# Optimization experiments

Hardware: AMD Instinct MI355X
Metric: run time of the kernel (lower is better)

## Reference

```python
import jax, jax.numpy as jnp
import numpy as np
from jax import lax


def _conv1x1(x, w, b=None):
    # x: [N,C,H,W], w: [O,C]
    y = jnp.einsum('nchw,oc->nohw', x, w)
    if b is not None:
        y = y + b[None, :, None, None]
    return y


def _bn(x, g, b, rm, rv):
    # eval-mode BatchNorm2d, eps=1e-5 (torch default)
    inv = g / jnp.sqrt(rv + 1e-5)
    return x * inv[None, :, None, None] + (b - rm * inv)[None, :, None, None]


def setup_inputs() -> dict:
    key = jax.random.key(0)
    ks = jax.random.split(key, 32)
    N, C1, C2, H, W = 16, 256, 256, 64, 64
    mid = C2 // 16  # local_att reduction=16
    f32 = jnp.float32
    def nrm(k, shp, s=0.05):
        return s * jax.random.normal(k, shp, f32)
    return dict(
        x1=jax.random.normal(ks[0], (N, C1, H, W), f32),
        x2=jax.random.normal(ks[1], (N, C2, H, W), f32),
        conv1_w=nrm(ks[2], (C2, C1)), conv1_b=nrm(ks[3], (C2,)),
        conv2_w=nrm(ks[4], (C2, C2)), conv2_b=nrm(ks[5], (C2,)),
        conv3_w=nrm(ks[6], (C2, C2)), conv3_b=nrm(ks[7], (C2,)),
        conv4_w=nrm(ks[8], (C2, C2)), conv4_b=nrm(ks[9], (C2,)),
        conv4g_w=nrm(ks[10], (1, C2)), conv4g_b=nrm(ks[11], (1,)),
        bn_g=1.0 + nrm(ks[12], (C2,)), bn_b=nrm(ks[13], (C2,)),
        bn_rm=nrm(ks[14], (C2,)), bn_rv=1.0 + 0.1 * jax.random.uniform(ks[15], (C2,), f32),
        gamma=jax.random.normal(ks[16], (C2, 1, 1), f32), beta=jnp.zeros((C2, 1, 1), f32),
        gate_w=nrm(ks[17], (C2, C2)), gate_b=nrm(ks[18], (C2,)),
        dw_w=nrm(ks[19], (C2, 1, 3, 3)), dw_b=nrm(ks[20], (C2,)),
        interact_w=nrm(ks[21], (C2 // 4, C2 // 4)), interact_b=0.5 + nrm(ks[22], (C2 // 4,)),
        ca_w=nrm(ks[23], (1, 1, 5)),  # channel_att conv1d kernel, k=5 for C=256
        la1_w=nrm(ks[24], (mid, C2)),
        la_bn_g=1.0 + nrm(ks[25], (mid,)), la_bn_b=nrm(ks[26], (mid,)),
        la_bn_rm=nrm(ks[27], (mid,)), la_bn_rv=1.0 + 0.1 * jax.random.uniform(ks[28], (mid,), f32),
        fh_w=nrm(ks[29], (C2, mid)), fw_w=nrm(ks[30], (C2, mid)),
    )


def reference(x1, x2, conv1_w, conv1_b, conv2_w, conv2_b, conv3_w, conv3_b,
              conv4_w, conv4_b, conv4g_w, conv4g_b, bn_g, bn_b, bn_rm, bn_rv,
              gamma, beta, gate_w, gate_b, dw_w, dw_b, interact_w, interact_b,
              ca_w, la1_w, la_bn_g, la_bn_b, la_bn_rm, la_bn_rv, fh_w, fw_w):
    N, _, H, W = x1.shape
    C = conv1_w.shape[0]
    g1 = _conv1x1(x1, conv1_w, conv1_b)
    w1 = jax.nn.sigmoid(_bn(g1, bn_g, bn_b, bn_rm, bn_rv))
    g2 = _conv1x1(x2, conv2_w, conv2_b)
    w2 = jax.nn.sigmoid(_bn(g2, bn_g, bn_b, bn_rm, bn_rv))
    XG = g1 + g2

    # channel_att: GAP -> conv1d(k=5) across channels -> sigmoid gate
    y = XG.mean((2, 3))[:, None, :]  # [N,1,C]
    y = lax.conv_general_dilated(y, ca_w, (1,), [(2, 2)],
                                 dimension_numbers=('NCH', 'OIH', 'NCH'))
    temp = XG * jax.nn.sigmoid(y[:, 0, :])[:, :, None, None]

    # spatial sigmoid gate then 4-way group interact + softmax reweight
    Xs = jax.nn.sigmoid(_conv1x1(XG, conv4g_w, conv4g_b)) * XG
    C4 = C // 4
    Xr = Xs.reshape(N, 4, C4, H, W)
    o1 = jnp.einsum('ngchw,oc->ngohw', Xr, interact_w) + interact_b[None, None, :, None, None]
    xmap = o1.reshape(N, 4, 1, C4 * H * W)
    xav = xmap / xmap.mean(-1, keepdims=True)
    soft = jax.nn.softmax(xav, axis=2)  # softmax over size-1 dim -> ones (faithful)
    out = (soft.reshape(N, 4, C4, H, W) * Xr).reshape(N, C, H, W)

    # per-group (16) normalization using X_GOBAL stats (std unbiased, ddof=1)
    GN = 16
    xs = XG.reshape(N, GN, -1)
    mu = xs.mean(-1, keepdims=True)
    sd = jnp.std(xs, axis=-1, keepdims=True, ddof=1)
    x_gui = ((out.reshape(N, GN, -1) - mu) / (sd + 1e-10)).reshape(N, C, H, W)
    x_gui = x_gui * gamma[None] + beta[None]

    # threshold masks vs global-avg sigmoid reweights
    rw = jax.nn.sigmoid(XG.mean((2, 3), keepdims=True))  # [N,C,1,1]
    up1 = rw >= w1
    up2 = rw >= w2
    zero = jnp.zeros((), XG.dtype)
    x_up = jnp.where(up1, XG, zero) + jnp.where(up2, XG, zero)
    x_low = jnp.where(~up1, XG, zero) + jnp.where(~up2, XG, zero)

    # low branch: dwconv3x3 -> 1x1 -> channel-softmax gate
    dw = lax.conv_general_dilated(x_low, dw_w, (1, 1), [(1, 1), (1, 1)],
                                  dimension_numbers=('NCHW', 'OIHW', 'NCHW'),
                                  feature_group_count=C) + dw_b[None, :, None, None]
    x11 = _conv1x1(dw, conv3_w, conv3_b)
    gate = jax.nn.softmax(jax.nn.relu(x_low.mean((2, 3)) @ gate_w.T + gate_b), axis=1)
    xL = x11 * gate[:, :, None, None] + _conv1x1(x_up, conv4_w, conv4_b) + x_gui + temp

    # local_att (coordinate attention)
    xh = jnp.swapaxes(xL.mean(3, keepdims=True), 2, 3)  # [N,C,1,H]
    xw = xL.mean(2, keepdims=True)                       # [N,C,1,W]
    yc = jax.nn.relu(_bn(_conv1x1(jnp.concatenate([xh, xw], 3), la1_w),
                         la_bn_g, la_bn_b, la_bn_rm, la_bn_rv))
    sh = jax.nn.sigmoid(_conv1x1(jnp.swapaxes(yc[..., :H], 2, 3), fh_w))  # [N,C,H,1]
    sw = jax.nn.sigmoid(_conv1x1(yc[..., H:], fw_w))                      # [N,C,1,W]
    return xL * sh * sw
```

## Files before the change

### kernel.cpp

```cpp
#include <hip/hip_runtime.h>
#include <cstddef>
#include <cstdint>

constexpr int NN = 16, CC = 256, HH = 64, WW = 64, HW = 64 * 64;
constexpr size_t FSZ = (size_t)NN * CC * HW;

typedef short bf16x8 __attribute__((ext_vector_type(8)));
typedef float f32x4 __attribute__((ext_vector_type(4)));

__device__ __forceinline__ float sigmoidf_(float x) { return 1.f / (1.f + expf(-x)); }

__device__ __forceinline__ unsigned short bf16_rne(float f) {
    uint32_t u = __builtin_bit_cast(uint32_t, f);
    u += 0x7FFFu + ((u >> 16) & 1u);
    return (unsigned short)(u >> 16);
}
__device__ __forceinline__ float bf16_tof(unsigned short h) {
    uint32_t u = ((uint32_t)h) << 16;
    return __builtin_bit_cast(float, u);
}

__global__ __launch_bounds__(256) void wsplit_kernel(
    const float* __restrict__ w1, const float* __restrict__ w2,
    const float* __restrict__ w3, const float* __restrict__ w4,
    unsigned short* __restrict__ w1h, unsigned short* __restrict__ w1m, unsigned short* __restrict__ w1l,
    unsigned short* __restrict__ w2h, unsigned short* __restrict__ w2m, unsigned short* __restrict__ w2l,
    unsigned short* __restrict__ w4h, unsigned short* __restrict__ w4l,
    unsigned short* __restrict__ w3b) {
    const int i = blockIdx.x * 256 + threadIdx.x;
    {
        float x = w1[i];
        unsigned short h = bf16_rne(x); float r = x - bf16_tof(h);
        unsigned short m = bf16_rne(r); float r2 = r - bf16_tof(m);
        w1h[i] = h; w1m[i] = m; w1l[i] = bf16_rne(r2);
    }
    {
        float x = w2[i];
        unsigned short h = bf16_rne(x); float r = x - bf16_tof(h);
        unsigned short m = bf16_rne(r); float r2 = r - bf16_tof(m);
        w2h[i] = h; w2m[i] = m; w2l[i] = bf16_rne(r2);
    }
    {
        float x = w4[i];
        unsigned short h = bf16_rne(x); float r = x - bf16_tof(h);
        w4h[i] = h; w4l[i] = bf16_rne(r);
    }
    w3b[i] = bf16_rne(w3[i]);
}

template <int NS>
__global__ __launch_bounds__(256) void tsplit_kernel(const float* __restrict__ X,
                                                     unsigned short* __restrict__ O0,
                                                     unsigned short* __restrict__ O1,
                                                     unsigned short* __restrict__ O2) {
    const int hw0 = blockIdx.x * 64, c0 = blockIdx.y * 64, n = blockIdx.z;
    __shared__ float sT[64][65];
    const int tid = threadIdx.x;
    {
        const int hwl = (tid & 15) << 2;
        const int cl = tid >> 4;
#pragma unroll
        for (int p = 0; p < 4; ++p) {
            const int c = cl + p * 16;
            const float4 v = *(const float4*)(X + ((size_t)(n * CC + c0 + c)) * HW + hw0 + hwl);
            sT[c][hwl] = v.x; sT[c][hwl + 1] = v.y; sT[c][hwl + 2] = v.z; sT[c][hwl + 3] = v.w;
        }
    }
    __syncthreads();
    const int hwl = tid >> 2, cb = (tid & 3) << 4;
    unsigned short h[16], m[16], l[16];
#pragma unroll
    for (int j = 0; j < 16; ++j) {
        const float x = sT[cb + j][hwl];
        const unsigned short hh = bf16_rne(x);
        h[j] = hh;
        if (NS >= 2) {
            const float r = x - bf16_tof(hh);
            const unsigned short mm = bf16_rne(r);
            m[j] = mm;
            if (NS >= 3) l[j] = bf16_rne(r - bf16_tof(mm));
        }
    }
    const size_t ob = ((size_t)(n * HW + hw0 + hwl)) * 256 + c0 + cb;
    *(int4*)(O0 + ob) = *(int4*)&h[0]; *(int4*)(O0 + ob + 8) = *(int4*)&h[8];
    if (NS >= 2) { *(int4*)(O1 + ob) = *(int4*)&m[0]; *(int4*)(O1 + ob + 8) = *(int4*)&m[8]; }
    if (NS >= 3) { *(int4*)(O2 + ob) = *(int4*)&l[0]; *(int4*)(O2 + ob + 8) = *(int4*)&l[8]; }
}

template <int NS>
__device__ __forceinline__ void mfma_core(const unsigned short* X0,
                                          const unsigned short* X1,
                                          const unsigned short* X2,
                                          const unsigned short* W0,
                                          const unsigned short* W1,
                                          const unsigned short* W2,
                                          int n, int hw0, int o0, f32x4 acc[4]) {
    __shared__ unsigned short sX[NS][64][40];
    __shared__ unsigned short sW[NS][64][40];
    const int tid = threadIdx.x;
    const int row = tid >> 2, koff = (tid & 3) << 3;
    const int lane = tid & 63, wv = tid >> 6, quad = lane >> 4, nlo = lane & 15;
    const unsigned short* Xs[3] = {X0, X1, X2};
    const unsigned short* Ws[3] = {W0, W1, W2};
    const size_t xbase = ((size_t)(n * HW + hw0 + row)) * 256 + koff;
    const size_t wbase = ((size_t)(o0 + row)) * 256 + koff;
    for (int k0 = 0; k0 < 256; k0 += 32) {
#pragma unroll
        for (int s = 0; s < NS; ++s) {
            *(int4*)&sX[s][row][koff] = *(const int4*)(Xs[s] + xbase + k0);
            *(int4*)&sW[s][row][koff] = *(const int4*)(Ws[s] + wbase + k0);
        }
        __syncthreads();
        bf16x8 af[NS];
#pragma unroll
        for (int s = 0; s < NS; ++s) af[s] = *(const bf16x8*)&sW[s][wv * 16 + nlo][quad * 8];
#pragma unroll
        for (int nt = 0; nt < 4; ++nt) {
            bf16x8 bfr[NS];
#pragma unroll
            for (int s = 0; s < NS; ++s) bfr[s] = *(const bf16x8*)&sX[s][nt * 16 + nlo][quad * 8];
            if (NS == 3) {
                acc[nt] = __builtin_amdgcn_mfma_f32_16x16x32_bf16(af[1], bfr[1], acc[nt], 0, 0, 0);
                acc[nt] = __builtin_amdgcn_mfma_f32_16x16x32_bf16(af[0], bfr[2], acc[nt], 0, 0, 0);
                acc[nt] = __builtin_amdgcn_mfma_f32_16x16x32_bf16(af[2], bfr[0], acc[nt], 0, 0, 0);
                acc[nt] = __builtin_amdgcn_mfma_f32_16x16x32_bf16(af[0], bfr[1], acc[nt], 0, 0, 0);
                acc[nt] = __builtin_amdgcn_mfma_f32_16x16x32_bf16(af[1], bfr[0], acc[nt], 0, 0, 0);
                acc[nt] = __builtin_amdgcn_mfma_f32_16x16x32_bf16(af[0], bfr[0], acc[nt], 0, 0, 0);
            } else if (NS == 2) {
                acc[nt] = __builtin_amdgcn_mfma_f32_16x16x32_bf16(af[0], bfr[1], acc[nt], 0, 0, 0);
                acc[nt] = __builtin_amdgcn_mfma_f32_16x16x32_bf16(af[1], bfr[0], acc[nt], 0, 0, 0);
                acc[nt] = __builtin_amdgcn_mfma_f32_16x16x32_bf16(af[0], bfr[0], acc[nt], 0, 0, 0);
            } else {
                acc[nt] = __builtin_amdgcn_mfma_f32_16x16x32_bf16(af[0], bfr[0], acc[nt], 0, 0, 0);
            }
        }
        __syncthreads();
    }
}

template <int NS>
__global__ __launch_bounds__(256) void gemm_mfma_kernel(
    const unsigned short* __restrict__ X0, const unsigned short* __restrict__ X1,
    const unsigned short* __restrict__ X2, const unsigned short* __restrict__ W0,
    const unsigned short* __restrict__ W1, const unsigned short* __restrict__ W2,
    const float* __restrict__ bias, float* __restrict__ Y) {
    const int hw0 = blockIdx.x * 64, o0 = blockIdx.y * 64, n = blockIdx.z;
    f32x4 acc[4] = {};
    mfma_core<NS>(X0, X1, X2, W0, W1, W2, n, hw0, o0, acc);
    const int lane = threadIdx.x & 63, wv = threadIdx.x >> 6;
    const int quad = lane >> 4, nlo = lane & 15;
    const int om = o0 + wv * 16 + quad * 4;
#pragma unroll
    for (int nt = 0; nt < 4; ++nt) {
        const int hw = hw0 + nt * 16 + nlo;
#pragma unroll
        for (int r = 0; r < 4; ++r) {
            const int o = om + r;
            Y[((size_t)(n * CC + o)) * HW + hw] = acc[nt][r] + bias[o];
        }
    }
}

__global__ __launch_bounds__(256) void gemm_final_kernel(
    const unsigned short* __restrict__ X0, const unsigned short* __restrict__ W0,
    const float* __restrict__ bias,
    const float* A, const float* __restrict__ XG, const float* __restrict__ s_pix,
    const float* __restrict__ gate, const float* __restrict__ ca_sig,
    const float* __restrict__ mu_g, const float* __restrict__ isd_g,
    const float* __restrict__ gamma, const float* __restrict__ beta,
    float* out) {
    const int hw0 = blockIdx.x * 64, o0 = blockIdx.y * 64, n = blockIdx.z;
    f32x4 acc[4] = {};
    mfma_core<1>(X0, nullptr, nullptr, W0, nullptr, nullptr, n, hw0, o0, acc);
    const int lane = threadIdx.x & 63, wv = threadIdx.x >> 6;
    const int quad = lane >> 4, nlo = lane & 15;
    const int om = o0 + wv * 16 + quad * 4;
#pragma unroll
    for (int nt = 0; nt < 4; ++nt) {
        const int hw = hw0 + nt * 16 + nlo;
        const int pix = n * HW + hw;
        const float sp = s_pix[pix];
#pragma unroll
        for (int r = 0; r < 4; ++r) {
            const int o = om + r;
            const float g = gate[n * CC + o];
            const float cs = ca_sig[n * CC + o];
            const float mu = mu_g[n * 16 + (o >> 4)];
            const float isd = isd_g[n * 16 + (o >> 4)];
            const size_t rowi = ((size_t)(n * CC + o)) * HW + hw;
            const float xg = XG[rowi];
            const float gui = (sp * xg - mu) * isd * gamma[o] + beta[o];
            out[rowi] = (acc[nt][r] + bias[o]) * g + A[rowi] + gui + xg * cs;
        }
    }
}

__global__ __launch_bounds__(256) void xg_stats_kernel(const float* __restrict__ g1,
                                                       const float* __restrict__ g2,
                                                       float* __restrict__ XG,
                                                       float* __restrict__ sum_c,
                                                       float* __restrict__ sq_c) {
    const size_t base = (size_t)blockIdx.x * HW;
    float s = 0.f, q = 0.f;
#pragma unroll 4
    for (int r = 0; r < 16; ++r) {
        const size_t i = base + threadIdx.x + r * 256;
        const float xg = g1[i] + g2[i];
        XG[i] = xg;
        s += xg;
        q += xg * xg;
    }
    __shared__ float sm[8];
    for (int off = 32; off; off >>= 1) { s += __shfl_down(s, off); q += __shfl_down(q, off); }
    const int w = threadIdx.x >> 6;
    if ((threadIdx.x & 63) == 0) { sm[w] = s; sm[4 + w] = q; }
    __syncthreads();
    if (threadIdx.x == 0) {
        sum_c[blockIdx.x] = sm[0] + sm[1] + sm[2] + sm[3];
        sq_c[blockIdx.x] = sm[4] + sm[5] + sm[6] + sm[7];
    }
}

__global__ __launch_bounds__(256) void stats2_kernel(const float* __restrict__ sum_c,
                                                     const float* __restrict__ sq_c,
                                                     const float* __restrict__ caw,
                                                     float* __restrict__ rw,
                                                     float* __restrict__ ca_sig,
                                                     float* __restrict__ mu_g,
                                                     float* __restrict__ isd_g) {
    const int n = blockIdx.x, c = threadIdx.x;
    __shared__ float m[256];
    const float mean = sum_c[n * CC + c] * (1.f / (float)HW);
    m[c] = mean;
    rw[n * CC + c] = sigmoidf_(mean);
    __syncthreads();
    float y = 0.f;
#pragma unroll
    for (int k = 0; k < 5; ++k) {
        const int cc = c - 2 + k;
        if (cc >= 0 && cc < 256) y += m[cc] * caw[k];
    }
    ca_sig[n * CC + c] = sigmoidf_(y);
    if (c < 16) {
        float S = 0.f, Q = 0.f;
        for (int j = 0; j < 16; ++j) {
            S += sum_c[n * CC + c * 16 + j];
            Q += sq_c[n * CC + c * 16 + j];
        }
        const float cnt = 65536.f;
        const float mu = S / cnt;
        float var = (Q - S * S / cnt) * (1.f / (cnt - 1.f));
        var = fmaxf(var, 0.f);
        mu_g[n * 16 + c] = mu;
        isd_g[n * 16 + c] = 1.f / (sqrtf(var) + 1e-10f);
    }
}

__global__ __launch_bounds__(256) void conv4g_kernel(const float* __restrict__ XG,
                                                     const float* __restrict__ cgw,
                                                     const float* __restrict__ cgb,
                                                     float* __restrict__ s_pix) {
    __shared__ float w[256];
    w[threadIdx.x] = cgw[threadIdx.x];
    __syncthreads();
    const int p = blockIdx.x * 256 + threadIdx.x;
    const int n = p >> 12, hw = p & 4095;
    const float* base = XG + (size_t)n * CC * HW + hw;
    float s = cgb[0];
#pragma unroll 8
    for (int c = 0; c < 256; ++c) s += base[(size_t)c * HW] * w[c];
    s_pix[p] = sigmoidf_(s);
}

__global__ __launch_bounds__(256) void masks_kernel(float* g1_xlow,
                                                    const float* __restrict__ g2,
                                                    const float* __restrict__ XG,
                                                    const float* __restrict__ rw,
                                                    const float* __restrict__ bng,
                                                    const float* __restrict__ bnb,
                                                    const float* __restrict__ bnrm,
                                                    const float* __restrict__ bnrv,
                                                    float* __restrict__ xup,
                                                    float* __restrict__ xlow_sum) {
    const int nc = blockIdx.x;
    const int c = nc & 255;
    const float inv = bng[c] / sqrtf(bnrv[c] + 1e-5f);
    const float off = bnb[c] - bnrm[c] * inv;
    const float rwv = rw[nc];
    const size_t base = (size_t)nc * HW;
    float lsum = 0.f;
#pragma unroll 4
    for (int r = 0; r < 16; ++r) {
        const size_t i = base + threadIdx.x + r * 256;
        const float a = g1_xlow[i];
        const float b = g2[i];
        const float xg = XG[i];
        const float w1 = sigmoidf_(inv * a + off);
        const float w2 = sigmoidf_(inv * b + off);
        const float cu = (rwv >= w1 ? 1.f : 0.f) + (rwv >= w2 ? 1.f : 0.f);
        xup[i] = xg * cu;
        const float xl = xg * (2.f - cu);
        g1_xlow[i] = xl;
        lsum += xl;
    }
    __shared__ float sm[4];
    for (int off2 = 32; off2; off2 >>= 1) lsum += __shfl_down(lsum, off2);
    if ((threadIdx.x & 63) == 0) sm[threadIdx.x >> 6] = lsum;
    __syncthreads();
    if (threadIdx.x == 0) xlow_sum[nc] = sm[0] + sm[1] + sm[2] + sm[3];
}

__global__ __launch_bounds__(256) void gate_kernel(const float* __restrict__ xlow_sum,
                                                   const float* __restrict__ gatew,
                                                   const float* __restrict__ gateb,
                                                   float* __restrict__ gate) {
    const int n = blockIdx.x, c = threadIdx.x;
    __shared__ float xm[256];
    __shared__ float red[256];
    xm[c] = xlow_sum[n * CC + c] * (1.f / (float)HW);
    __syncthreads();
    float acc = gateb[c];
    const float* wr = gatew + (size_t)c * 256;
#pragma unroll 8
    for (int k = 0; k < 256; ++k) acc += xm[k] * wr[k];
    const float v = fmaxf(acc, 0.f);
    red[c] = v;
    __syncthreads();
    for (int s = 128; s > 0; s >>= 1) {
        if (c < s) red[c] = fmaxf(red[c], red[c + s]);
        __syncthreads();
    }
    const float mx = red[0];
    __syncthreads();
    const float e = expf(v - mx);
    red[c] = e;
    __syncthreads();
    for (int s = 128; s > 0; s >>= 1) {
        if (c < s) red[c] += red[c + s];
        __syncthreads();
    }
    gate[n * CC + c] = e / red[0];
}

__global__ __launch_bounds__(256) void dwconv_kernel(const float* __restrict__ xlow,
                                                     const float* __restrict__ dww,
                                                     const float* __restrict__ dwb,
                                                     float* __restrict__ out) {
    const int c = blockIdx.x & 255;
    __shared__ float sl[64][65];
    const size_t base = (size_t)blockIdx.x * HW;
    for (int r = 0; r < 16; ++r) {
        const int idx = threadIdx.x + r * 256;
        sl[idx >> 6][idx & 63] = xlow[base + idx];
    }
    float wk[9];
#pragma unroll
    for (int j = 0; j < 9; ++j) wk[j] = dww[c * 9 + j];
    const float bias = dwb[c];
    __syncthreads();
    for (int r = 0; r < 16; ++r) {
        const int idx = threadIdx.x + r * 256;
        const int h = idx >> 6, w = idx & 63;
        float acc = bias;
#pragma unroll
        for (int dh = 0; dh < 3; ++dh) {
            const int hh = h + dh - 1;
            if (hh < 0 || hh > 63) continue;
#pragma unroll
            for (int dw2 = 0; dw2 < 3; ++dw2) {
                const int ww2 = w + dw2 - 1;
                if (ww2 < 0 || ww2 > 63) continue;
                acc += sl[hh][ww2] * wk[dh * 3 + dw2];
            }
        }
        out[base + idx] = acc;
    }
}

__global__ __launch_bounds__(256) void pool_kernel(const float* __restrict__ xL,
                                                   float* __restrict__ xh,
                                                   float* __restrict__ xw) {
    __shared__ float sl[64][65];
    const size_t base = (size_t)blockIdx.x * HW;
    for (int r = 0; r < 16; ++r) {
        const int idx = threadIdx.x + r * 256;
        sl[idx >> 6][idx & 63] = xL[base + idx];
    }
    __syncthreads();
    const int t = threadIdx.x;
    if (t < 64) {
        float s = 0.f;
        for (int w = 0; w < 64; ++w) s += sl[t][w];
        xh[(size_t)blockIdx.x * 64 + t] = s * (1.f / 64.f);
    } else if (t < 128) {
        const int w = t - 64;
        float s = 0.f;
        for (int h = 0; h < 64; ++h) s += sl[h][w];
        xw[(size_t)blockIdx.x * 64 + w] = s * (1.f / 64.f);
    }
}

__global__ __launch_bounds__(256) void local_att_kernel(const float* __restrict__ xh,
                                                        const float* __restrict__ xw,
                                                        const float* __restrict__ la1w,
                                                        const float* __restrict__ lag,
                                                        const float* __restrict__ lab,
                                                        const float* __restrict__ larm,
                                                        const float* __restrict__ larv,
                                                        const float* __restrict__ fhw,
                                                        const float* __restrict__ fww,
                                                        float* __restrict__ sh,
                                                        float* __restrict__ sw) {
    const int n = blockIdx.x;
    __shared__ float w1s[16 * 256];
    __shared__ float fhs[256 * 16];
    __shared__ float fws[256 * 16];
    __shared__ float ycs[16][128];
    for (int i = threadIdx.x; i < 4096; i += 256) {
        w1s[i] = la1w[i];
        fhs[i] = fhw[i];
        fws[i] = fww[i];
    }
    __syncthreads();
    for (int idx = threadIdx.x; idx < 2048; idx += 256) {
        const int m = idx >> 7, p = idx & 127;
        const float* vsrc = (p < 64) ? (xh + (size_t)n * CC * 64 + p)
                                     : (xw + (size_t)n * CC * 64 + (p - 64));
        float acc = 0.f;
#pragma unroll 8
        for (int c = 0; c < 256; ++c) acc += w1s[m * 256 + c] * vsrc[(size_t)c * 64];
        const float inv = lag[m] / sqrtf(larv[m] + 1e-5f);
        const float off = lab[m] - larm[m] * inv;
        ycs[m][p] = fmaxf(inv * acc + off, 0.f);
    }
    __syncthreads();
    for (int idx = threadIdx.x; idx < 16384; idx += 256) {
        const int c = idx >> 6, h = idx & 63;
        float a1 = 0.f, a2 = 0.f;
#pragma unroll
        for (int m = 0; m < 16; ++m) {
            a1 += fhs[c * 16 + m] * ycs[m][h];
            a2 += fws[c * 16 + m] * ycs[m][64 + h];
        }
        sh[(size_t)n * CC * 64 + idx] = sigmoidf_(a1);
        sw[(size_t)n * CC * 64 + idx] = sigmoidf_(a2);
    }
}

__global__ __launch_bounds__(256) void final_kernel(float* __restrict__ out,
                                                    const float* __restrict__ sh,
                                                    const float* __restrict__ sw) {
    __shared__ float shs[64], sws[64];
    const int t = threadIdx.x;
    if (t < 64) shs[t] = sh[(size_t)blockIdx.x * 64 + t];
    else if (t < 128) sws[t - 64] = sw[(size_t)blockIdx.x * 64 + (t - 64)];
    __syncthreads();
    const size_t base = (size_t)blockIdx.x * HW;
#pragma unroll 4
    for (int r = 0; r < 16; ++r) {
        const int idx = t + r * 256;
        out[base + idx] *= shs[idx >> 6] * sws[idx & 63];
    }
}

extern "C" void kernel_launch(void* const* d_in, const int* in_sizes, int n_in,
                              void* d_out, int out_size, void* d_ws, size_t ws_size,
                              hipStream_t stream) {
    const float* x1 = (const float*)d_in[0];
    const float* x2 = (const float*)d_in[1];
    const float* c1w = (const float*)d_in[2];
    const float* c1b = (const float*)d_in[3];
    const float* c2w = (const float*)d_in[4];
    const float* c2b = (const float*)d_in[5];
    const float* c3w = (const float*)d_in[6];
    const float* c3b = (const float*)d_in[7];
    const float* c4w = (const float*)d_in[8];
    const float* c4b = (const float*)d_in[9];
    const float* cgw = (const float*)d_in[10];
    const float* cgb = (const float*)d_in[11];
    const float* bng = (const float*)d_in[12];
    const float* bnb = (const float*)d_in[13];
    const float* bnrm = (const float*)d_in[14];
    const float* bnrv = (const float*)d_in[15];
    const float* gamma = (const float*)d_in[16];
    const float* beta = (const float*)d_in[17];
    const float* gatew = (const float*)d_in[18];
    const float* gateb = (const float*)d_in[19];
    const float* dww = (const float*)d_in[20];
    const float* dwb = (const float*)d_in[21];
    const float* caw = (const float*)d_in[24];
    const float* la1w = (const float*)d_in[25];
    const float* lag = (const float*)d_in[26];
    const float* lab = (const float*)d_in[27];
    const float* larm = (const float*)d_in[28];
    const float* larv = (const float*)d_in[29];
    const float* fhw = (const float*)d_in[30];
    const float* fww = (const float*)d_in[31];

    float* ws = (float*)d_ws;
    float* buf0 = ws;
    float* buf1 = ws + FSZ;
    float* buf2 = ws + 2 * FSZ;
    float* sp = ws + 3 * FSZ;
    float* sum_c = sp;    sp += 4096;
    float* sq_c = sp;     sp += 4096;
    float* rw = sp;       sp += 4096;
    float* ca_sig = sp;   sp += 4096;
    float* xlow_sum = sp; sp += 4096;
    float* mu_g = sp;     sp += 256;
    float* isd_g = sp;    sp += 256;
    float* s_pix = sp;    sp += (size_t)NN * HW;
    float* xh = sp;       sp += (size_t)NN * CC * 64;
    float* xwb = sp;      sp += (size_t)NN * CC * 64;
    float* shb = sp;      sp += (size_t)NN * CC * 64;
    float* swb = sp;      sp += (size_t)NN * CC * 64;
    unsigned short* wsp = (unsigned short*)shb;
    unsigned short* w1h = wsp + 0 * 65536;
    unsigned short* w1m = wsp + 1 * 65536;
    unsigned short* w1l = wsp + 2 * 65536;
    unsigned short* w2h = wsp + 3 * 65536;
    unsigned short* w2m = wsp + 4 * 65536;
    unsigned short* w2l = wsp + 5 * 65536;
    unsigned short* w4h = wsp + 6 * 65536;
    unsigned short* w4l = wsp + 7 * 65536;
    unsigned short* w3b = wsp + 8 * 65536;

    float* out = (float*)d_out;

    const dim3 gg(HW / 64, CC / 64, NN);

    wsplit_kernel<<<256, 256, 0, stream>>>(c1w, c2w, c3w, c4w, w1h, w1m, w1l,
                                           w2h, w2m, w2l, w4h, w4l, w3b);
    {
        unsigned short* sx0 = (unsigned short*)buf1;
        unsigned short* sx1 = (unsigned short*)buf1 + FSZ;
        unsigned short* sx2 = (unsigned short*)buf2;
        tsplit_kernel<3><<<gg, 256, 0, stream>>>(x1, sx0, sx1, sx2);
        gemm_mfma_kernel<3><<<gg, 256, 0, stream>>>(sx0, sx1, sx2, w1h, w1m, w1l, c1b, buf0);
    }
    {
        unsigned short* sx0 = (unsigned short*)out;
        unsigned short* sx1 = (unsigned short*)out + FSZ;
        unsigned short* sx2 = (unsigned short*)buf2;
        tsplit_kernel<3><<<gg, 256, 0, stream>>>(x2, sx0, sx1, sx2);
        gemm_mfma_kernel<3><<<gg, 256, 0, stream>>>(sx0, sx1, sx2, w2h, w2m, w2l, c2b, buf1);
    }
    xg_stats_kernel<<<NN * CC, 256, 0, stream>>>(buf0, buf1, buf2, sum_c, sq_c);
    stats2_kernel<<<NN, 256, 0, stream>>>(sum_c, sq_c, caw, rw, ca_sig, mu_g, isd_g);
    conv4g_kernel<<<NN * HW / 256, 256, 0, stream>>>(buf2, cgw, cgb, s_pix);
    masks_kernel<<<NN * CC, 256, 0, stream>>>(buf0, buf1, buf2, rw, bng, bnb, bnrm, bnrv,
                                              out, xlow_sum);
    float* gate = sum_c;
    gate_kernel<<<NN, 256, 0, stream>>>(xlow_sum, gatew, gateb, gate);
    dwconv_kernel<<<NN * CC, 256, 0, stream>>>(buf0, dww, dwb, buf1);
    {
        unsigned short* sx0 = (unsigned short*)buf0;
        unsigned short* sx1 = (unsigned short*)buf0 + FSZ;
        tsplit_kernel<2><<<gg, 256, 0, stream>>>(out, sx0, sx1, nullptr);
        gemm_mfma_kernel<2><<<gg, 256, 0, stream>>>(sx0, sx1, nullptr, w4h, w4l, nullptr,
                                                    c4b, out);
    }
    {
        unsigned short* sx0 = (unsigned short*)buf0;
        tsplit_kernel<1><<<gg, 256, 0, stream>>>(buf1, sx0, nullptr, nullptr);
        gemm_final_kernel<<<gg, 256, 0, stream>>>(sx0, w3b, c3b, out, buf2, s_pix,
                                                  gate, ca_sig, mu_g, isd_g, gamma, beta, out);
    }
    pool_kernel<<<NN * CC, 256, 0, stream>>>(out, xh, xwb);
    local_att_kernel<<<NN, 256, 0, stream>>>(xh, xwb, la1w, lag, lab, larm, larv,
                                             fhw, fww, shb, swb);
    final_kernel<<<NN * CC, 256, 0, stream>>>(out, shb, swb);
}
```

Measured before the change: 782.6 us.

## Widen GEMM output tiles and fuse mask computation with bf16 splitting

The MFMA GEMM core now computes 128 output channels per block instead of 64, so each X tile loaded into shared memory feeds twice as many MFMAs. Launch bounds request three blocks per SM. The masks kernel is replaced by a tiled version that writes the x_up hi/lo bf16 split directly and accumulates the x_low sums with atomics, with zero-initialisation moved into stats2. This drops the fp32 x_up round trip and one tsplit pass, at the cost of more registers and LDS per GEMM block, fewer blocks in the grid, and atomics on the reduction.

```diff
diff --git a/kernel.cpp b/kernel.cpp
--- a/kernel.cpp
+++ b/kernel.cpp
@@ -88,50 +88,57 @@
 }
 
 template <int NS>
-__device__ __forceinline__ void mfma_core(const unsigned short* X0,
-                                          const unsigned short* X1,
-                                          const unsigned short* X2,
-                                          const unsigned short* W0,
-                                          const unsigned short* W1,
-                                          const unsigned short* W2,
-                                          int n, int hw0, int o0, f32x4 acc[4]) {
+__device__ __forceinline__ void mfma_core2(const unsigned short* X0,
+                                           const unsigned short* X1,
+                                           const unsigned short* X2,
+                                           const unsigned short* W0,
+                                           const unsigned short* W1,
+                                           const unsigned short* W2,
+                                           int n, int hw0, int o0, f32x4 (&acc)[2][4]) {
     __shared__ unsigned short sX[NS][64][40];
-    __shared__ unsigned short sW[NS][64][40];
+    __shared__ unsigned short sW[NS][128][40];
     const int tid = threadIdx.x;
-    const int row = tid >> 2, koff = (tid & 3) << 3;
     const int lane = tid & 63, wv = tid >> 6, quad = lane >> 4, nlo = lane & 15;
+    const int srow = tid >> 2, skoff = (tid & 3) << 3;
     const unsigned short* Xs[3] = {X0, X1, X2};
     const unsigned short* Ws[3] = {W0, W1, W2};
-    const size_t xbase = ((size_t)(n * HW + hw0 + row)) * 256 + koff;
-    const size_t wbase = ((size_t)(o0 + row)) * 256 + koff;
+    const size_t xg = ((size_t)(n * HW + hw0 + srow)) * 256 + skoff;
+    const size_t wg = ((size_t)(o0 + srow)) * 256 + skoff;
     for (int k0 = 0; k0 < 256; k0 += 32) {
 #pragma unroll
         for (int s = 0; s < NS; ++s) {
-            *(int4*)&sX[s][row][koff] = *(const int4*)(Xs[s] + xbase + k0);
-            *(int4*)&sW[s][row][koff] = *(const int4*)(Ws[s] + wbase + k0);
+            *(int4*)&sX[s][srow][skoff] = *(const int4*)(Xs[s] + xg + k0);
+            *(int4*)&sW[s][srow][skoff] = *(const int4*)(Ws[s] + wg + k0);
+            *(int4*)&sW[s][64 + srow][skoff] = *(const int4*)(Ws[s] + wg + 64 * 256 + k0);
         }
         __syncthreads();
-        bf16x8 af[NS];
-#pragma unroll
-        for (int s = 0; s < NS; ++s) af[s] = *(const bf16x8*)&sW[s][wv * 16 + nlo][quad * 8];
+        bf16x8 af[NS][2];
+#pragma unroll
+        for (int s = 0; s < NS; ++s) {
+            af[s][0] = *(const bf16x8*)&sW[s][wv * 16 + nlo][quad * 8];
+            af[s][1] = *(const bf16x8*)&sW[s][64 + wv * 16 + nlo][quad * 8];
+        }
 #pragma unroll
         for (int nt = 0; nt < 4; ++nt) {
             bf16x8 bfr[NS];
 #pragma unroll
             for (int s = 0; s < NS; ++s) bfr[s] = *(const bf16x8*)&sX[s][nt * 16 + nlo][quad * 8];
-            if (NS == 3) {
-                acc[nt] = __builtin_amdgcn_mfma_f32_16x16x32_bf16(af[1], bfr[1], acc[nt], 0, 0, 0);
-                acc[nt] = __builtin_amdgcn_mfma_f32_16x16x32_bf16(af[0], bfr[2], acc[nt], 0, 0, 0);
-                acc[nt] = __builtin_amdgcn_mfma_f32_16x16x32_bf16(af[2], bfr[0], acc[nt], 0, 0, 0);
-                acc[nt] = __builtin_amdgcn_mfma_f32_16x16x32_bf16(af[0], bfr[1], acc[nt], 0, 0, 0);
-                acc[nt] = __builtin_amdgcn_mfma_f32_16x16x32_bf16(af[1], bfr[0], acc[nt], 0, 0, 0);
-                acc[nt] = __builtin_amdgcn_mfma_f32_16x16x32_bf16(af[0], bfr[0], acc[nt], 0, 0, 0);
-            } else if (NS == 2) {
-                acc[nt] = __builtin_amdgcn_mfma_f32_16x16x32_bf16(af[0], bfr[1], acc[nt], 0, 0, 0);
-                acc[nt] = __builtin_amdgcn_mfma_f32_16x16x32_bf16(af[1], bfr[0], acc[nt], 0, 0, 0);
-                acc[nt] = __builtin_amdgcn_mfma_f32_16x16x32_bf16(af[0], bfr[0], acc[nt], 0, 0, 0);
-            } else {
-                acc[nt] = __builtin_amdgcn_mfma_f32_16x16x32_bf16(af[0], bfr[0], acc[nt], 0, 0, 0);
+#pragma unroll
+            for (int f = 0; f < 2; ++f) {
+                if (NS == 3) {
+                    acc[f][nt] = __builtin_amdgcn_mfma_f32_16x16x32_bf16(af[1][f], bfr[1], acc[f][nt], 0, 0, 0);
+                    acc[f][nt] = __builtin_amdgcn_mfma_f32_16x16x32_bf16(af[0][f], bfr[2], acc[f][nt], 0, 0, 0);
+                    acc[f][nt] = __builtin_amdgcn_mfma_f32_16x16x32_bf16(af[2][f], bfr[0], acc[f][nt], 0, 0, 0);
+                    acc[f][nt] = __builtin_amdgcn_mfma_f32_16x16x32_bf16(af[0][f], bfr[1], acc[f][nt], 0, 0, 0);
+                    acc[f][nt] = __builtin_amdgcn_mfma_f32_16x16x32_bf16(af[1][f], bfr[0], acc[f][nt], 0, 0, 0);
+                    acc[f][nt] = __builtin_amdgcn_mfma_f32_16x16x32_bf16(af[0][f], bfr[0], acc[f][nt], 0, 0, 0);
+                } else if (NS == 2) {
+                    acc[f][nt] = __builtin_amdgcn_mfma_f32_16x16x32_bf16(af[0][f], bfr[1], acc[f][nt], 0, 0, 0);
+                    acc[f][nt] = __builtin_amdgcn_mfma_f32_16x16x32_bf16(af[1][f], bfr[0], acc[f][nt], 0, 0, 0);
+                    acc[f][nt] = __builtin_amdgcn_mfma_f32_16x16x32_bf16(af[0][f], bfr[0], acc[f][nt], 0, 0, 0);
+                } else {
+                    acc[f][nt] = __builtin_amdgcn_mfma_f32_16x16x32_bf16(af[0][f], bfr[0], acc[f][nt], 0, 0, 0);
+                }
             }
         }
         __syncthreads();
@@ -139,58 +146,64 @@
 }
 
 template <int NS>
-__global__ __launch_bounds__(256) void gemm_mfma_kernel(
+__global__ __launch_bounds__(256, 3) void gemm_mfma_kernel(
     const unsigned short* __restrict__ X0, const unsigned short* __restrict__ X1,
     const unsigned short* __restrict__ X2, const unsigned short* __restrict__ W0,
     const unsigned short* __restrict__ W1, const unsigned short* __restrict__ W2,
     const float* __restrict__ bias, float* __restrict__ Y) {
-    const int hw0 = blockIdx.x * 64, o0 = blockIdx.y * 64, n = blockIdx.z;
-    f32x4 acc[4] = {};
-    mfma_core<NS>(X0, X1, X2, W0, W1, W2, n, hw0, o0, acc);
+    const int hw0 = blockIdx.x * 64, o0 = blockIdx.y * 128, n = blockIdx.z;
+    f32x4 acc[2][4] = {};
+    mfma_core2<NS>(X0, X1, X2, W0, W1, W2, n, hw0, o0, acc);
     const int lane = threadIdx.x & 63, wv = threadIdx.x >> 6;
     const int quad = lane >> 4, nlo = lane & 15;
-    const int om = o0 + wv * 16 + quad * 4;
-#pragma unroll
-    for (int nt = 0; nt < 4; ++nt) {
-        const int hw = hw0 + nt * 16 + nlo;
-#pragma unroll
-        for (int r = 0; r < 4; ++r) {
-            const int o = om + r;
-            Y[((size_t)(n * CC + o)) * HW + hw] = acc[nt][r] + bias[o];
-        }
-    }
-}
-
-__global__ __launch_bounds__(256) void gemm_final_kernel(
+#pragma unroll
+    for (int f = 0; f < 2; ++f) {
+        const int om = o0 + f * 64 + wv * 16 + quad * 4;
+#pragma unroll
+        for (int nt = 0; nt < 4; ++nt) {
+            const int hw = hw0 + nt * 16 + nlo;
+#pragma unroll
+            for (int r = 0; r < 4; ++r) {
+                const int o = om + r;
+                Y[((size_t)(n * CC + o)) * HW + hw] = acc[f][nt][r] + bias[o];
+            }
+        }
+    }
+}
+
+__global__ __launch_bounds__(256, 3) void gemm_final_kernel(
     const unsigned short* __restrict__ X0, const unsigned short* __restrict__ W0,
     const float* __restrict__ bias,
-    const float* A, const float* __restrict__ XG, const float* __restrict__ s_pix,
+    const float* __restrict__ A, const float* __restrict__ XG, const float* __restrict__ s_pix,
     const float* __restrict__ gate, const float* __restrict__ ca_sig,
     const float* __restrict__ mu_g, const float* __restrict__ isd_g,
     const float* __restrict__ gamma, const float* __restrict__ beta,
-    float* out) {
-    const int hw0 = blockIdx.x * 64, o0 = blockIdx.y * 64, n = blockIdx.z;
-    f32x4 acc[4] = {};
-    mfma_core<1>(X0, nullptr, nullptr, W0, nullptr, nullptr, n, hw0, o0, acc);
+    float* __restrict__ out) {
+    const int hw0 = blockIdx.x * 64, o0 = blockIdx.y * 128, n = blockIdx.z;
+    f32x4 acc[2][4] = {};
+    mfma_core2<1>(X0, nullptr, nullptr, W0, nullptr, nullptr, n, hw0, o0, acc);
     const int lane = threadIdx.x & 63, wv = threadIdx.x >> 6;
     const int quad = lane >> 4, nlo = lane & 15;
-    const int om = o0 + wv * 16 + quad * 4;
-#pragma unroll
-    for (int nt = 0; nt < 4; ++nt) {
-        const int hw = hw0 + nt * 16 + nlo;
-        const int pix = n * HW + hw;
-        const float sp = s_pix[pix];
-#pragma unroll
-        for (int r = 0; r < 4; ++r) {
-            const int o = om + r;
-            const float g = gate[n * CC + o];
-            const float cs = ca_sig[n * CC + o];
-            const float mu = mu_g[n * 16 + (o >> 4)];
-            const float isd = isd_g[n * 16 + (o >> 4)];
-            const size_t rowi = ((size_t)(n * CC + o)) * HW + hw;
-            const float xg = XG[rowi];
-            const float gui = (sp * xg - mu) * isd * gamma[o] + beta[o];
-            out[rowi] = (acc[nt][r] + bias[o]) * g + A[rowi] + gui + xg * cs;
+#pragma unroll
+    for (int f = 0; f < 2; ++f) {
+        const int om = o0 + f * 64 + wv * 16 + quad * 4;
+#pragma unroll
+        for (int nt = 0; nt < 4; ++nt) {
+            const int hw = hw0 + nt * 16 + nlo;
+            const int pix = n * HW + hw;
+            const float sp = s_pix[pix];
+#pragma unroll
+            for (int r = 0; r < 4; ++r) {
+                const int o = om + r;
+                const float g = gate[n * CC + o];
+                const float cs = ca_sig[n * CC + o];
+                const float mu = mu_g[n * 16 + (o >> 4)];
+                const float isd = isd_g[n * 16 + (o >> 4)];
+                const size_t rowi = ((size_t)(n * CC + o)) * HW + hw;
+                const float xg = XG[rowi];
+                const float gui = (sp * xg - mu) * isd * gamma[o] + beta[o];
+                out[rowi] = (acc[f][nt][r] + bias[o]) * g + A[rowi] + gui + xg * cs;
+            }
         }
     }
 }
@@ -227,12 +240,14 @@
                                                      float* __restrict__ rw,
                                                      float* __restrict__ ca_sig,
                                                      float* __restrict__ mu_g,
-                                                     float* __restrict__ isd_g) {
+                                                     float* __restrict__ isd_g,
+                                                     float* __restrict__ xlow_sum) {
     const int n = blockIdx.x, c = threadIdx.x;
     __shared__ float m[256];
     const float mean = sum_c[n * CC + c] * (1.f / (float)HW);
     m[c] = mean;
     rw[n * CC + c] = sigmoidf_(mean);
+    xlow_sum[n * CC + c] = 0.f;
     __syncthreads();
     float y = 0.f;
 #pragma unroll
@@ -272,42 +287,64 @@
     s_pix[p] = sigmoidf_(s);
 }
 
-__global__ __launch_bounds__(256) void masks_kernel(float* g1_xlow,
-                                                    const float* __restrict__ g2,
-                                                    const float* __restrict__ XG,
-                                                    const float* __restrict__ rw,
-                                                    const float* __restrict__ bng,
-                                                    const float* __restrict__ bnb,
-                                                    const float* __restrict__ bnrm,
-                                                    const float* __restrict__ bnrv,
-                                                    float* __restrict__ xup,
-                                                    float* __restrict__ xlow_sum) {
-    const int nc = blockIdx.x;
-    const int c = nc & 255;
+__global__ __launch_bounds__(256) void masks_split_kernel(
+    float* g1_xlow,
+    const float* __restrict__ g2,
+    const float* __restrict__ XG,
+    const float* __restrict__ rw,
+    const float* __restrict__ bng, const float* __restrict__ bnb,
+    const float* __restrict__ bnrm, const float* __restrict__ bnrv,
+    unsigned short* __restrict__ O0, unsigned short* __restrict__ O1,
+    float* __restrict__ xlow_sum) {
+    const int hw0 = blockIdx.x * 64, c0 = blockIdx.y * 64, n = blockIdx.z;
+    __shared__ float sT[64][65];
+    const int tid = threadIdx.x;
+    const int cl = tid >> 2;
+    const int q = tid & 3;
+    const int c = c0 + cl;
     const float inv = bng[c] / sqrtf(bnrv[c] + 1e-5f);
     const float off = bnb[c] - bnrm[c] * inv;
-    const float rwv = rw[nc];
-    const size_t base = (size_t)nc * HW;
+    const float rwv = rw[n * CC + c];
+    const size_t rowb = ((size_t)(n * CC + c)) * HW + hw0;
     float lsum = 0.f;
-#pragma unroll 4
-    for (int r = 0; r < 16; ++r) {
-        const size_t i = base + threadIdx.x + r * 256;
-        const float a = g1_xlow[i];
-        const float b = g2[i];
-        const float xg = XG[i];
-        const float w1 = sigmoidf_(inv * a + off);
-        const float w2 = sigmoidf_(inv * b + off);
-        const float cu = (rwv >= w1 ? 1.f : 0.f) + (rwv >= w2 ? 1.f : 0.f);
-        xup[i] = xg * cu;
-        const float xl = xg * (2.f - cu);
-        g1_xlow[i] = xl;
-        lsum += xl;
-    }
-    __shared__ float sm[4];
-    for (int off2 = 32; off2; off2 >>= 1) lsum += __shfl_down(lsum, off2);
-    if ((threadIdx.x & 63) == 0) sm[threadIdx.x >> 6] = lsum;
-    __syncthreads();
-    if (threadIdx.x == 0) xlow_sum[nc] = sm[0] + sm[1] + sm[2] + sm[3];
+#pragma unroll
+    for (int j = 0; j < 4; ++j) {
+        const int hwl = q * 4 + j * 16;
+        const float4 a = *(const float4*)(g1_xlow + rowb + hwl);
+        const float4 b = *(const float4*)(g2 + rowb + hwl);
+        const float4 x = *(const float4*)(XG + rowb + hwl);
+        const float* ap = &a.x; const float* bp = &b.x; const float* xp = &x.x;
+        float4 xlv;
+        float* xlp = &xlv.x;
+#pragma unroll
+        for (int e = 0; e < 4; ++e) {
+            const float w1 = sigmoidf_(inv * ap[e] + off);
+            const float w2 = sigmoidf_(inv * bp[e] + off);
+            const float cu = (rwv >= w1 ? 1.f : 0.f) + (rwv >= w2 ? 1.f : 0.f);
+            const float xu = xp[e] * cu;
+            const float xl = xp[e] * (2.f - cu);
+            sT[cl][hwl + e] = xu;
+            xlp[e] = xl;
+            lsum += xl;
+        }
+        *(float4*)(g1_xlow + rowb + hwl) = xlv;
+    }
+    lsum += __shfl_xor(lsum, 1);
+    lsum += __shfl_xor(lsum, 2);
+    if (q == 0) atomicAdd(&xlow_sum[n * CC + c], lsum);
+    __syncthreads();
+    const int hwl2 = tid >> 2, cb = (tid & 3) << 4;
+    unsigned short h[16], m[16];
+#pragma unroll
+    for (int j = 0; j < 16; ++j) {
+        const float x = sT[cb + j][hwl2];
+        const unsigned short hh = bf16_rne(x);
+        h[j] = hh;
+        m[j] = bf16_rne(x - bf16_tof(hh));
+    }
+    const size_t ob = ((size_t)(n * HW + hw0 + hwl2)) * 256 + c0 + cb;
+    *(int4*)(O0 + ob) = *(int4*)&h[0]; *(int4*)(O0 + ob + 8) = *(int4*)&h[8];
+    *(int4*)(O1 + ob) = *(int4*)&m[0]; *(int4*)(O1 + ob + 8) = *(int4*)&m[8];
 }
 
 __global__ __launch_bounds__(256) void gate_kernel(const float* __restrict__ xlow_sum,
@@ -527,7 +564,8 @@
 
     float* out = (float*)d_out;
 
-    const dim3 gg(HW / 64, CC / 64, NN);
+    const dim3 gt(HW / 64, CC / 64, NN);
+    const dim3 gg(HW / 64, CC / 128, NN);
 
     wsplit_kernel<<<256, 256, 0, stream>>>(c1w, c2w, c3w, c4w, w1h, w1m, w1l,
                                            w2h, w2m, w2l, w4h, w4l, w3b);
@@ -535,35 +573,41 @@
         unsigned short* sx0 = (unsigned short*)buf1;
         unsigned short* sx1 = (unsigned short*)buf1 + FSZ;
         unsigned short* sx2 = (unsigned short*)buf2;
-        tsplit_kernel<3><<<gg, 256, 0, stream>>>(x1, sx0, sx1, sx2);
+        tsplit_kernel<3><<<gt, 256, 0, stream>>>(x1, sx0, sx1, sx2);
         gemm_mfma_kernel<3><<<gg, 256, 0, stream>>>(sx0, sx1, sx2, w1h, w1m, w1l, c1b, buf0);
     }
     {
         unsigned short* sx0 = (unsigned short*)out;
         unsigned short* sx1 = (unsigned short*)out + FSZ;
         unsigned short* sx2 = (unsigned short*)buf2;
-        tsplit_kernel<3><<<gg, 256, 0, stream>>>(x2, sx0, sx1, sx2);
+        tsplit_kernel<3><<<gt, 256, 0, stream>>>(x2, sx0, sx1, sx2);
         gemm_mfma_kernel<3><<<gg, 256, 0, stream>>>(sx0, sx1, sx2, w2h, w2m, w2l, c2b, buf1);
     }
     xg_stats_kernel<<<NN * CC, 256, 0, stream>>>(buf0, buf1, buf2, sum_c, sq_c);
-    stats2_kernel<<<NN, 256, 0, stream>>>(sum_c, sq_c, caw, rw, ca_sig, mu_g, isd_g);
+    stats2_kernel<<<NN, 256, 0, stream>>>(sum_c, sq_c, caw, rw, ca_sig, mu_g, isd_g, xlow_sum);
     conv4g_kernel<<<NN * HW / 256, 256, 0, stream>>>(buf2, cgw, cgb, s_pix);
-    masks_kernel<<<NN * CC, 256, 0, stream>>>(buf0, buf1, buf2, rw, bng, bnb, bnrm, bnrv,
-                                              out, xlow_sum);
+    {
+        unsigned short* ux0 = (unsigned short*)out;
+        unsigned short* ux1 = (unsigned short*)out + FSZ;
+        masks_split_kernel<<<gt, 256, 0, stream>>>(buf0, buf1, buf2, rw, bng, bnb, bnrm, bnrv,
+                                                   ux0, ux1, xlow_sum);
+    }
     float* gate = sum_c;
     gate_kernel<<<NN, 256, 0, stream>>>(xlow_sum, gatew, gateb, gate);
     dwconv_kernel<<<NN * CC, 256, 0, stream>>>(buf0, dww, dwb, buf1);
     {
         unsigned short* sx0 = (unsigned short*)buf0;
-        unsigned short* sx1 = (unsigned short*)buf0 + FSZ;
-        tsplit_kernel<2><<<gg, 256, 0, stream>>>(out, sx0, sx1, nullptr);
-        gemm_mfma_kernel<2><<<gg, 256, 0, stream>>>(sx0, sx1, nullptr, w4h, w4l, nullptr,
-                                                    c4b, out);
+        tsplit_kernel<1><<<gt, 256, 0, stream>>>(buf1, sx0, nullptr, nullptr);
+    }
+    {
+        unsigned short* ux0 = (unsigned short*)out;
+        unsigned short* ux1 = (unsigned short*)out + FSZ;
+        gemm_mfma_kernel<2><<<gg, 256, 0, stream>>>(ux0, ux1, nullptr, w4h, w4l, nullptr,
+                                                    c4b, buf1);
     }
     {
         unsigned short* sx0 = (unsigned short*)buf0;
-        tsplit_kernel<1><<<gg, 256, 0, stream>>>(buf1, sx0, nullptr, nullptr);
-        gemm_final_kernel<<<gg, 256, 0, stream>>>(sx0, w3b, c3b, out, buf2, s_pix,
+        gemm_final_kernel<<<gg, 256, 0, stream>>>(sx0, w3b, c3b, buf1, buf2, s_pix,
                                                   gate, ca_sig, mu_g, isd_g, gamma, beta, out);
     }
     pool_kernel<<<NN * CC, 256, 0, stream>>>(out, xh, xwb);
```

Result: faster. 729.4 us (-6.8%).
